# Optimization experiments

Measured on AMD Instinct MI355X. Metric: run time of the kernel, lower is better.

The kernel has to match this reference:

```python
import jax, jax.numpy as jnp
import numpy as np

WIDTH = 64
HEIGHT = 64
FEAT = 128
LAT = 64
NUM_SLOTS = 7


def pixel_coords(img_size):
    g = jnp.linspace(-1.0, 1.0, img_size)
    g1, g2 = jnp.meshgrid(g, g, indexing='ij')  # matches torch.meshgrid default
    return jnp.stack([g1, g2], axis=0)[None]  # (1, 2, S, S)


def clamp_pg(x, lo, hi):
    # clamp that preserves gradients (straight-through)
    return x + jax.lax.stop_gradient(jnp.clip(x, lo, hi) - x)


def setup_inputs() -> dict:
    key = jax.random.key(0)
    k0, k1, k2, k3 = jax.random.split(key, 4)
    bs = 64
    x = jax.random.normal(k0, (bs, FEAT, WIDTH, HEIGHT), jnp.float32)
    rand_pixel = jax.random.uniform(k1, (bs, 1, WIDTH, HEIGHT), jnp.float32)
    conv_w = jax.random.normal(k2, (LAT, FEAT), jnp.float32) / np.sqrt(FEAT)
    conv_b = jax.random.normal(k3, (LAT,), jnp.float32) * 0.01
    gate = jnp.asarray(0.5, jnp.float32)  # ScalarGate parameter (nonzero so c_f is non-degenerate)
    # laplacian kernel: sigma_init = 1 / (sqrt(num_slots) * log 2)
    log_sigma = jnp.asarray(np.log(1.0 / (np.sqrt(NUM_SLOTS) * np.log(2.0))), jnp.float32)
    return {'x': x, 'rand_pixel': rand_pixel, 'conv_w': conv_w, 'conv_b': conv_b,
            'gate': gate, 'log_sigma': log_sigma, 'num_cl_steps': 6}


def _forward(x, rand_pixel, conv_w, conv_b, gate, log_sigma, num_cl_steps):
    bs = x.shape[0]
    # SemiConv: gated 1x1 conv + fixed uv coordinate channels
    out = gate * (jnp.einsum('of,bfhw->bohw', conv_w, x) + conv_b[None, :, None, None])
    uv = jnp.concatenate([jnp.zeros((1, LAT - 2, WIDTH, HEIGHT), out.dtype),
                          pixel_coords(WIDTH).astype(out.dtype)], axis=1)
    c_f = out + uv                      # (bs, LAT, W, H)
    delta = out[:, -2:]                 # (bs, 2, W, H)
    sigma = jnp.exp(log_sigma)
    c_flat = c_f.reshape(bs, LAT, -1)   # (bs, LAT, W*H)
    b_idx = jnp.arange(bs)
    log_s0 = jnp.zeros((bs, 1, WIDTH, HEIGHT), c_f.dtype)

    def step(log_s, _):
        # interpolate-to-same-size is identity -> scope = exp(log_s)
        probs = (rand_pixel * jnp.exp(log_s)).reshape(bs, -1)
        idx = jnp.argmax(probs, axis=1)                 # (bs,)
        seed = c_flat[b_idx, :, idx]                    # (bs, LAT)
        diff = c_f - seed[:, :, None, None]
        dist = jnp.sqrt(clamp_pg((diff ** 2).sum(1), 1e-10, 1e10))  # euclidian (laplacian kernel)
        alpha = jnp.exp(-dist / sigma)[:, None]         # (bs, 1, W, H)
        alpha = clamp_pg(alpha, 0.01, 0.99)
        log_m = log_s + jnp.log(alpha)
        new_log_s = log_s + jnp.log1p(-alpha)
        return new_log_s, (log_m, new_log_s, seed)

    log_s_final, (log_m_steps, log_s_steps, seeds) = jax.lax.scan(
        step, log_s0, None, length=num_cl_steps)
    # log_m_k has num_cl_steps masks plus the final scope appended
    log_m_k = jnp.concatenate([log_m_steps, log_s_final[None]], axis=0)
    log_s_k = jnp.concatenate([log_s0[None], log_s_steps], axis=0)
    return log_m_k, log_s_k, c_f, delta, seeds


def reference(x, rand_pixel, conv_w, conv_b, gate, log_sigma, num_cl_steps):
    return _forward(x, rand_pixel, conv_w, conv_b, gate, log_sigma, num_cl_steps)
```

## Files before the change

### kernel.cpp

```cpp
#include <hip/hip_runtime.h>

#define NPIX 4096
#define FEAT 128
#define LAT 64
#define BS 64
#define NSTEPS 6

#define OFF_LOGM  0u
#define OFF_LOGS  1835008u
#define OFF_CF    3670016u
#define OFF_DELTA 20447232u
#define OFF_SEEDS 20971520u

__device__ __forceinline__ void amax_comb(float& bv, int& bi, float v, int i) {
    if (v > bv || (v == bv && i < bi)) { bv = v; bi = i; }
}

__global__ __launch_bounds__(256, 2) void conv_kernel(
    const float* __restrict__ x, const float* __restrict__ rand_pixel,
    const float* __restrict__ w, const float* __restrict__ bias,
    const float* __restrict__ gate_p, float* __restrict__ out,
    float* __restrict__ pval, int* __restrict__ pidx)
{
    __shared__ float wT[FEAT][68];

    const int tid  = threadIdx.x;
    const int b    = blockIdx.x >> 4;
    const int tile = blockIdx.x & 15;
    const int p0   = tile * 256;
    const int lane = tid & 63;
    const int og   = tid >> 6;

    #pragma unroll
    for (int k = 0; k < 32; ++k) {
        int idx = k * 256 + tid;
        wT[idx & 127][idx >> 7] = w[idx];
    }
    __syncthreads();

    const float gate = gate_p[0];

    float4 acc[16];
    #pragma unroll
    for (int i = 0; i < 16; ++i) acc[i] = make_float4(0.f, 0.f, 0.f, 0.f);

    const float* xb = x + (size_t)b * FEAT * NPIX + p0 + lane * 4;

    #pragma unroll 2
    for (int f = 0; f < FEAT; ++f) {
        float4 xv = *(const float4*)(xb + (size_t)f * NPIX);
        const float* wrow = &wT[f][og * 16];
        #pragma unroll
        for (int oi = 0; oi < 16; oi += 4) {
            float4 wv = *(const float4*)(wrow + oi);
            acc[oi+0].x = fmaf(wv.x, xv.x, acc[oi+0].x);
            acc[oi+0].y = fmaf(wv.x, xv.y, acc[oi+0].y);
            acc[oi+0].z = fmaf(wv.x, xv.z, acc[oi+0].z);
            acc[oi+0].w = fmaf(wv.x, xv.w, acc[oi+0].w);
            acc[oi+1].x = fmaf(wv.y, xv.x, acc[oi+1].x);
            acc[oi+1].y = fmaf(wv.y, xv.y, acc[oi+1].y);
            acc[oi+1].z = fmaf(wv.y, xv.z, acc[oi+1].z);
            acc[oi+1].w = fmaf(wv.y, xv.w, acc[oi+1].w);
            acc[oi+2].x = fmaf(wv.z, xv.x, acc[oi+2].x);
            acc[oi+2].y = fmaf(wv.z, xv.y, acc[oi+2].y);
            acc[oi+2].z = fmaf(wv.z, xv.z, acc[oi+2].z);
            acc[oi+2].w = fmaf(wv.z, xv.w, acc[oi+2].w);
            acc[oi+3].x = fmaf(wv.w, xv.x, acc[oi+3].x);
            acc[oi+3].y = fmaf(wv.w, xv.y, acc[oi+3].y);
            acc[oi+3].z = fmaf(wv.w, xv.z, acc[oi+3].z);
            acc[oi+3].w = fmaf(wv.w, xv.w, acc[oi+3].w);
        }
    }

    const int pbase = p0 + lane * 4;
    float* cf = out + OFF_CF + (size_t)b * LAT * NPIX;

    #pragma unroll
    for (int oi = 0; oi < 16; ++oi) {
        int o = og * 16 + oi;
        float bo = bias[o];
        float4 v;
        v.x = gate * (acc[oi].x + bo);
        v.y = gate * (acc[oi].y + bo);
        v.z = gate * (acc[oi].z + bo);
        v.w = gate * (acc[oi].w + bo);
        if (o >= 62) {
            float* dp = out + OFF_DELTA + ((size_t)b * 2 + (o - 62)) * NPIX + pbase;
            *(float4*)dp = v;
            if (o == 62) {
                float g1 = (float)(-1.0 + 2.0 * (double)(pbase >> 6) / 63.0);
                v.x += g1; v.y += g1; v.z += g1; v.w += g1;
            } else {
                int j = pbase & 63;
                v.x += (float)(-1.0 + 2.0 * (double)(j + 0) / 63.0);
                v.y += (float)(-1.0 + 2.0 * (double)(j + 1) / 63.0);
                v.z += (float)(-1.0 + 2.0 * (double)(j + 2) / 63.0);
                v.w += (float)(-1.0 + 2.0 * (double)(j + 3) / 63.0);
            }
        }
        *(float4*)(cf + (size_t)o * NPIX + pbase) = v;
    }

    if (og == 0) {
        *(float4*)(out + OFF_LOGS + (size_t)b * NPIX + pbase) = make_float4(0.f, 0.f, 0.f, 0.f);

        float4 rv = *(const float4*)(rand_pixel + (size_t)b * NPIX + pbase);
        float bv = rv.x; int bi = pbase;
        if (rv.y > bv) { bv = rv.y; bi = pbase + 1; }
        if (rv.z > bv) { bv = rv.z; bi = pbase + 2; }
        if (rv.w > bv) { bv = rv.w; bi = pbase + 3; }
        #pragma unroll
        for (int off = 32; off > 0; off >>= 1) {
            float ov = __shfl_down(bv, off, 64);
            int   oi2 = __shfl_down(bi, off, 64);
            amax_comb(bv, bi, ov, oi2);
        }
        if (lane == 0) { pval[blockIdx.x] = bv; pidx[blockIdx.x] = bi; }
    }
}

__global__ __launch_bounds__(256, 4) void step_kernel(
    const float* __restrict__ rand_pixel, const float* __restrict__ log_sigma_p,
    float* __restrict__ out, float* __restrict__ pval, int* __restrict__ pidx,
    int step)
{
    __shared__ float s_seed[LAT];
    __shared__ float s_rv[4];
    __shared__ int   s_ri[4];

    const int tid  = threadIdx.x;
    const int b    = blockIdx.x >> 4;
    const int tile = blockIdx.x & 15;
    const int p    = tile * 256 + tid;

    float bv = -1.0f; int bi = 0;
    #pragma unroll
    for (int k = 0; k < 16; ++k) {
        float v = pval[b * 16 + k];
        int  id = pidx[b * 16 + k];
        amax_comb(bv, bi, v, id);
    }

    const float* cf = out + OFF_CF + (size_t)b * LAT * NPIX;
    if (tid < LAT) s_seed[tid] = cf[(size_t)tid * NPIX + bi];
    __syncthreads();

    if (tile == 0 && tid < LAT)
        out[OFF_SEEDS + ((size_t)step * BS + b) * LAT + tid] = s_seed[tid];

    float d2 = 0.f;
    #pragma unroll 16
    for (int c = 0; c < LAT; ++c) {
        float d = cf[(size_t)c * NPIX + p] - s_seed[c];
        d2 = fmaf(d, d, d2);
    }
    float dist  = sqrtf(fminf(fmaxf(d2, 1e-10f), 1e10f));
    float sigma = expf(log_sigma_p[0]);
    float alpha = expf(-dist / sigma);
    alpha = fminf(fmaxf(alpha, 0.01f), 0.99f);

    float ls  = out[OFF_LOGS + ((size_t)step * BS + b) * NPIX + p];
    float lm  = ls + logf(alpha);
    float lsn = ls + log1pf(-alpha);

    out[OFF_LOGM + ((size_t)step * BS + b) * NPIX + p]       = lm;
    out[OFF_LOGS + ((size_t)(step + 1) * BS + b) * NPIX + p] = lsn;
    if (step == NSTEPS - 1)
        out[OFF_LOGM + ((size_t)NSTEPS * BS + b) * NPIX + p] = lsn;

    if (step < NSTEPS - 1) {
        float prob = rand_pixel[(size_t)b * NPIX + p] * expf(lsn);
        int   idx  = p;
        #pragma unroll
        for (int off = 32; off > 0; off >>= 1) {
            float ov = __shfl_down(prob, off, 64);
            int   oi = __shfl_down(idx, off, 64);
            amax_comb(prob, idx, ov, oi);
        }
        int lane = tid & 63, wid = tid >> 6;
        if (lane == 0) { s_rv[wid] = prob; s_ri[wid] = idx; }
        __syncthreads();
        if (tid == 0) {
            float fb = s_rv[0]; int fi = s_ri[0];
            #pragma unroll
            for (int k = 1; k < 4; ++k) amax_comb(fb, fi, s_rv[k], s_ri[k]);
            pval[blockIdx.x] = fb; pidx[blockIdx.x] = fi;
        }
    }
}

extern "C" void kernel_launch(void* const* d_in, const int* in_sizes, int n_in,
                              void* d_out, int out_size, void* d_ws, size_t ws_size,
                              hipStream_t stream) {
    const float* x          = (const float*)d_in[0];
    const float* rand_pixel = (const float*)d_in[1];
    const float* w          = (const float*)d_in[2];
    const float* bias       = (const float*)d_in[3];
    const float* gate       = (const float*)d_in[4];
    const float* log_sigma  = (const float*)d_in[5];

    float* out  = (float*)d_out;
    float* pval = (float*)d_ws;
    int*   pidx = (int*)((char*)d_ws + 1024 * sizeof(float));

    conv_kernel<<<1024, 256, 0, stream>>>(x, rand_pixel, w, bias, gate, out, pval, pidx);
    for (int s = 0; s < NSTEPS; ++s)
        step_kernel<<<1024, 256, 0, stream>>>(rand_pixel, log_sigma, out, pval, pidx, s);
}
```

Baseline: 155.8 us.

## Fuse conv and clustering steps into one cooperative kernel with register-resident features

```diff
diff --git a/kernel.cpp b/kernel.cpp
--- a/kernel.cpp
+++ b/kernel.cpp
@@ -16,175 +16,170 @@
     if (v > bv || (v == bv && i < bi)) { bv = v; bi = i; }
 }
 
-__global__ __launch_bounds__(256, 2) void conv_kernel(
+__global__ void prep(const float* __restrict__ w, const float* __restrict__ bias,
+                     const float* __restrict__ gate_p,
+                     float* __restrict__ gwt, float* __restrict__ gbias,
+                     int* __restrict__ cnt)
+{
+    int i = blockIdx.x * 256 + threadIdx.x;
+    int o = i >> 7, f = i & 127;
+    gwt[f * 64 + o] = gate_p[0] * w[i];
+    if (i < 64)     gbias[i] = gate_p[0] * bias[i];
+    if (i < BS * 8) cnt[i]   = 0;
+}
+
+__global__ __launch_bounds__(512, 4) void fused(
     const float* __restrict__ x, const float* __restrict__ rand_pixel,
-    const float* __restrict__ w, const float* __restrict__ bias,
-    const float* __restrict__ gate_p, float* __restrict__ out,
-    float* __restrict__ pval, int* __restrict__ pidx)
+    const float* __restrict__ log_sigma_p, float* __restrict__ out,
+    const float* __restrict__ gwt, const float* __restrict__ gbias,
+    float* pv, int* pi, int* cnt)
 {
-    __shared__ float wT[FEAT][68];
+    __shared__ float s_mv[8];
+    __shared__ int   s_mi[8];
+    __shared__ __align__(16) float s_seed[LAT];
+    __shared__ float s_rv[8];
+    __shared__ int   s_ri[8];
 
     const int tid  = threadIdx.x;
-    const int b    = blockIdx.x >> 4;
-    const int tile = blockIdx.x & 15;
-    const int p0   = tile * 256;
-    const int lane = tid & 63;
-    const int og   = tid >> 6;
-
+    const int b    = blockIdx.x >> 3;
+    const int tile = blockIdx.x & 7;
+    const int p    = tile * 512 + tid;
+
+    const float* xr = x + (size_t)b * FEAT * NPIX + p;
+
+    float cr[LAT];
     #pragma unroll
-    for (int k = 0; k < 32; ++k) {
-        int idx = k * 256 + tid;
-        wT[idx & 127][idx >> 7] = w[idx];
-    }
-    __syncthreads();
-
-    const float gate = gate_p[0];
-
-    float4 acc[16];
+    for (int c = 0; c < LAT; ++c) cr[c] = gbias[c];
+
+    #pragma unroll 1
+    for (int fc = 0; fc < 8; ++fc) {
+        float xb[16];
+        #pragma unroll
+        for (int i = 0; i < 16; ++i)
+            xb[i] = xr[(size_t)(fc * 16 + i) * NPIX];
+        #pragma unroll
+        for (int f = 0; f < 16; ++f) {
+            const float* wr = gwt + (fc * 16 + f) * 64;
+            const float xv = xb[f];
+            #pragma unroll
+            for (int c = 0; c < LAT; ++c)
+                cr[c] = fmaf(wr[c], xv, cr[c]);
+        }
+    }
+
+    out[OFF_DELTA + ((size_t)b * 2 + 0) * NPIX + p] = cr[62];
+    out[OFF_DELTA + ((size_t)b * 2 + 1) * NPIX + p] = cr[63];
+    cr[62] += (float)(-1.0 + 2.0 * (double)(p >> 6) / 63.0);
+    cr[63] += (float)(-1.0 + 2.0 * (double)(p & 63) / 63.0);
+
+    float* cf = out + OFF_CF + (size_t)b * LAT * NPIX;
     #pragma unroll
-    for (int i = 0; i < 16; ++i) acc[i] = make_float4(0.f, 0.f, 0.f, 0.f);
-
-    const float* xb = x + (size_t)b * FEAT * NPIX + p0 + lane * 4;
-
-    #pragma unroll 2
-    for (int f = 0; f < FEAT; ++f) {
-        float4 xv = *(const float4*)(xb + (size_t)f * NPIX);
-        const float* wrow = &wT[f][og * 16];
-        #pragma unroll
-        for (int oi = 0; oi < 16; oi += 4) {
-            float4 wv = *(const float4*)(wrow + oi);
-            acc[oi+0].x = fmaf(wv.x, xv.x, acc[oi+0].x);
-            acc[oi+0].y = fmaf(wv.x, xv.y, acc[oi+0].y);
-            acc[oi+0].z = fmaf(wv.x, xv.z, acc[oi+0].z);
-            acc[oi+0].w = fmaf(wv.x, xv.w, acc[oi+0].w);
-            acc[oi+1].x = fmaf(wv.y, xv.x, acc[oi+1].x);
-            acc[oi+1].y = fmaf(wv.y, xv.y, acc[oi+1].y);
-            acc[oi+1].z = fmaf(wv.y, xv.z, acc[oi+1].z);
-            acc[oi+1].w = fmaf(wv.y, xv.w, acc[oi+1].w);
-            acc[oi+2].x = fmaf(wv.z, xv.x, acc[oi+2].x);
-            acc[oi+2].y = fmaf(wv.z, xv.y, acc[oi+2].y);
-            acc[oi+2].z = fmaf(wv.z, xv.z, acc[oi+2].z);
-            acc[oi+2].w = fmaf(wv.z, xv.w, acc[oi+2].w);
-            acc[oi+3].x = fmaf(wv.w, xv.x, acc[oi+3].x);
-            acc[oi+3].y = fmaf(wv.w, xv.y, acc[oi+3].y);
-            acc[oi+3].z = fmaf(wv.w, xv.z, acc[oi+3].z);
-            acc[oi+3].w = fmaf(wv.w, xv.w, acc[oi+3].w);
-        }
-    }
-
-    const int pbase = p0 + lane * 4;
-    float* cf = out + OFF_CF + (size_t)b * LAT * NPIX;
-
+    for (int c = 0; c < LAT; ++c) cf[(size_t)c * NPIX + p] = cr[c];
+
+    out[OFF_LOGS + (size_t)b * NPIX + p] = 0.f;
+
+    float cr2 = 0.f;
     #pragma unroll
-    for (int oi = 0; oi < 16; ++oi) {
-        int o = og * 16 + oi;
-        float bo = bias[o];
-        float4 v;
-        v.x = gate * (acc[oi].x + bo);
-        v.y = gate * (acc[oi].y + bo);
-        v.z = gate * (acc[oi].z + bo);
-        v.w = gate * (acc[oi].w + bo);
-        if (o >= 62) {
-            float* dp = out + OFF_DELTA + ((size_t)b * 2 + (o - 62)) * NPIX + pbase;
-            *(float4*)dp = v;
-            if (o == 62) {
-                float g1 = (float)(-1.0 + 2.0 * (double)(pbase >> 6) / 63.0);
-                v.x += g1; v.y += g1; v.z += g1; v.w += g1;
-            } else {
-                int j = pbase & 63;
-                v.x += (float)(-1.0 + 2.0 * (double)(j + 0) / 63.0);
-                v.y += (float)(-1.0 + 2.0 * (double)(j + 1) / 63.0);
-                v.z += (float)(-1.0 + 2.0 * (double)(j + 2) / 63.0);
-                v.w += (float)(-1.0 + 2.0 * (double)(j + 3) / 63.0);
-            }
-        }
-        *(float4*)(cf + (size_t)o * NPIX + pbase) = v;
-    }
-
-    if (og == 0) {
-        *(float4*)(out + OFF_LOGS + (size_t)b * NPIX + pbase) = make_float4(0.f, 0.f, 0.f, 0.f);
-
-        float4 rv = *(const float4*)(rand_pixel + (size_t)b * NPIX + pbase);
-        float bv = rv.x; int bi = pbase;
-        if (rv.y > bv) { bv = rv.y; bi = pbase + 1; }
-        if (rv.z > bv) { bv = rv.z; bi = pbase + 2; }
-        if (rv.w > bv) { bv = rv.w; bi = pbase + 3; }
+    for (int c = 0; c < LAT; ++c) cr2 = fmaf(cr[c], cr[c], cr2);
+
+    const float rp = rand_pixel[(size_t)b * NPIX + p];
+
+    {
+        float bv = rp; int bi = p;
         #pragma unroll
         for (int off = 32; off > 0; off >>= 1) {
             float ov = __shfl_down(bv, off, 64);
-            int   oi2 = __shfl_down(bi, off, 64);
-            amax_comb(bv, bi, ov, oi2);
-        }
-        if (lane == 0) { pval[blockIdx.x] = bv; pidx[blockIdx.x] = bi; }
-    }
-}
-
-__global__ __launch_bounds__(256, 4) void step_kernel(
-    const float* __restrict__ rand_pixel, const float* __restrict__ log_sigma_p,
-    float* __restrict__ out, float* __restrict__ pval, int* __restrict__ pidx,
-    int step)
-{
-    __shared__ float s_seed[LAT];
-    __shared__ float s_rv[4];
-    __shared__ int   s_ri[4];
-
-    const int tid  = threadIdx.x;
-    const int b    = blockIdx.x >> 4;
-    const int tile = blockIdx.x & 15;
-    const int p    = tile * 256 + tid;
-
-    float bv = -1.0f; int bi = 0;
-    #pragma unroll
-    for (int k = 0; k < 16; ++k) {
-        float v = pval[b * 16 + k];
-        int  id = pidx[b * 16 + k];
-        amax_comb(bv, bi, v, id);
-    }
-
-    const float* cf = out + OFF_CF + (size_t)b * LAT * NPIX;
-    if (tid < LAT) s_seed[tid] = cf[(size_t)tid * NPIX + bi];
-    __syncthreads();
-
-    if (tile == 0 && tid < LAT)
-        out[OFF_SEEDS + ((size_t)step * BS + b) * LAT + tid] = s_seed[tid];
-
-    float d2 = 0.f;
-    #pragma unroll 16
-    for (int c = 0; c < LAT; ++c) {
-        float d = cf[(size_t)c * NPIX + p] - s_seed[c];
-        d2 = fmaf(d, d, d2);
-    }
-    float dist  = sqrtf(fminf(fmaxf(d2, 1e-10f), 1e10f));
-    float sigma = expf(log_sigma_p[0]);
-    float alpha = expf(-dist / sigma);
-    alpha = fminf(fmaxf(alpha, 0.01f), 0.99f);
-
-    float ls  = out[OFF_LOGS + ((size_t)step * BS + b) * NPIX + p];
-    float lm  = ls + logf(alpha);
-    float lsn = ls + log1pf(-alpha);
-
-    out[OFF_LOGM + ((size_t)step * BS + b) * NPIX + p]       = lm;
-    out[OFF_LOGS + ((size_t)(step + 1) * BS + b) * NPIX + p] = lsn;
-    if (step == NSTEPS - 1)
-        out[OFF_LOGM + ((size_t)NSTEPS * BS + b) * NPIX + p] = lsn;
-
-    if (step < NSTEPS - 1) {
-        float prob = rand_pixel[(size_t)b * NPIX + p] * expf(lsn);
-        int   idx  = p;
-        #pragma unroll
-        for (int off = 32; off > 0; off >>= 1) {
-            float ov = __shfl_down(prob, off, 64);
-            int   oi = __shfl_down(idx, off, 64);
-            amax_comb(prob, idx, ov, oi);
+            int   oi = __shfl_down(bi, off, 64);
+            amax_comb(bv, bi, ov, oi);
         }
         int lane = tid & 63, wid = tid >> 6;
-        if (lane == 0) { s_rv[wid] = prob; s_ri[wid] = idx; }
+        if (lane == 0) { s_rv[wid] = bv; s_ri[wid] = bi; }
         __syncthreads();
         if (tid == 0) {
             float fb = s_rv[0]; int fi = s_ri[0];
             #pragma unroll
-            for (int k = 1; k < 4; ++k) amax_comb(fb, fi, s_rv[k], s_ri[k]);
-            pval[blockIdx.x] = fb; pidx[blockIdx.x] = fi;
+            for (int k = 1; k < 8; ++k) amax_comb(fb, fi, s_rv[k], s_ri[k]);
+            __hip_atomic_store(&pv[(0 * BS + b) * 8 + tile], fb,
+                               __ATOMIC_RELAXED, __HIP_MEMORY_SCOPE_AGENT);
+            __hip_atomic_store(&pi[(0 * BS + b) * 8 + tile], fi,
+                               __ATOMIC_RELAXED, __HIP_MEMORY_SCOPE_AGENT);
+            __hip_atomic_fetch_add(&cnt[b * 8 + 0], 1,
+                                   __ATOMIC_RELEASE, __HIP_MEMORY_SCOPE_AGENT);
+        }
+    }
+
+    const float sigma = expf(log_sigma_p[0]);
+    float ls = 0.f;
+
+    #pragma unroll 1
+    for (int s = 0; s < NSTEPS; ++s) {
+        if (tid == 0) {
+            while (__hip_atomic_load(&cnt[b * 8 + s], __ATOMIC_ACQUIRE,
+                                     __HIP_MEMORY_SCOPE_AGENT) < 8)
+                __builtin_amdgcn_s_sleep(2);
+        }
+        __syncthreads();
+        if (tid < 8) {
+            s_mv[tid] = __hip_atomic_load(&pv[(s * BS + b) * 8 + tid],
+                                          __ATOMIC_RELAXED, __HIP_MEMORY_SCOPE_AGENT);
+            s_mi[tid] = __hip_atomic_load(&pi[(s * BS + b) * 8 + tid],
+                                          __ATOMIC_RELAXED, __HIP_MEMORY_SCOPE_AGENT);
+        }
+        __syncthreads();
+
+        float bv = -1.0f; int bi = 0;
+        #pragma unroll
+        for (int k = 0; k < 8; ++k) amax_comb(bv, bi, s_mv[k], s_mi[k]);
+
+        if (tid < LAT) s_seed[tid] = cf[(size_t)tid * NPIX + bi];
+        __syncthreads();
+        if (tile == 0 && tid < LAT)
+            out[OFF_SEEDS + ((size_t)s * BS + b) * LAT + tid] = s_seed[tid];
+
+        float dot = 0.f, s2 = 0.f;
+        #pragma unroll
+        for (int c = 0; c < LAT; ++c) {
+            float sv = s_seed[c];
+            dot = fmaf(cr[c], sv, dot);
+            s2  = fmaf(sv, sv, s2);
+        }
+        float d2 = cr2 + s2 - 2.0f * dot;
+
+        float dist  = sqrtf(fminf(fmaxf(d2, 1e-10f), 1e10f));
+        float alpha = expf(-dist / sigma);
+        alpha = fminf(fmaxf(alpha, 0.01f), 0.99f);
+        float lm  = ls + logf(alpha);
+        float lsn = ls + log1pf(-alpha);
+
+        out[OFF_LOGM + ((size_t)s * BS + b) * NPIX + p]       = lm;
+        out[OFF_LOGS + ((size_t)(s + 1) * BS + b) * NPIX + p] = lsn;
+        ls = lsn;
+
+        if (s == NSTEPS - 1) {
+            out[OFF_LOGM + ((size_t)NSTEPS * BS + b) * NPIX + p] = lsn;
+        } else {
+            float prob = rp * expf(lsn);
+            int   idx  = p;
+            #pragma unroll
+            for (int off = 32; off > 0; off >>= 1) {
+                float ov = __shfl_down(prob, off, 64);
+                int   oi = __shfl_down(idx, off, 64);
+                amax_comb(prob, idx, ov, oi);
+            }
+            int lane = tid & 63, wid = tid >> 6;
+            if (lane == 0) { s_rv[wid] = prob; s_ri[wid] = idx; }
+            __syncthreads();
+            if (tid == 0) {
+                float fb = s_rv[0]; int fi = s_ri[0];
+                #pragma unroll
+                for (int k = 1; k < 8; ++k) amax_comb(fb, fi, s_rv[k], s_ri[k]);
+                __hip_atomic_store(&pv[((s + 1) * BS + b) * 8 + tile], fb,
+                                   __ATOMIC_RELAXED, __HIP_MEMORY_SCOPE_AGENT);
+                __hip_atomic_store(&pi[((s + 1) * BS + b) * 8 + tile], fi,
+                                   __ATOMIC_RELAXED, __HIP_MEMORY_SCOPE_AGENT);
+                __hip_atomic_fetch_add(&cnt[b * 8 + s + 1], 1,
+                                       __ATOMIC_RELEASE, __HIP_MEMORY_SCOPE_AGENT);
+            }
         }
     }
 }
@@ -199,11 +194,24 @@
     const float* gate       = (const float*)d_in[4];
     const float* log_sigma  = (const float*)d_in[5];
 
-    float* out  = (float*)d_out;
-    float* pval = (float*)d_ws;
-    int*   pidx = (int*)((char*)d_ws + 1024 * sizeof(float));
-
-    conv_kernel<<<1024, 256, 0, stream>>>(x, rand_pixel, w, bias, gate, out, pval, pidx);
-    for (int s = 0; s < NSTEPS; ++s)
-        step_kernel<<<1024, 256, 0, stream>>>(rand_pixel, log_sigma, out, pval, pidx, s);
-}
+    float* out = (float*)d_out;
+    float* gwt   = (float*)d_ws;
+    float* gbias = (float*)((char*)d_ws + 32768);
+    float* pv    = (float*)((char*)d_ws + 33024);
+    int*   pi    = (int*)((char*)d_ws + 45312);
+    int*   cnt   = (int*)((char*)d_ws + 57600);
+
+    prep<<<32, 256, 0, stream>>>(w, bias, gate, gwt, gbias, cnt);
+
+    const float* a0 = x; const float* a1 = rand_pixel; const float* a2 = log_sigma;
+    float* a3 = out; const float* a4 = gwt; const float* a5 = gbias;
+    float* a6 = pv; int* a7 = pi; int* a8 = cnt;
+    void* kp[9] = {(void*)&a0, (void*)&a1, (void*)&a2, (void*)&a3, (void*)&a4,
+                   (void*)&a5, (void*)&a6, (void*)&a7, (void*)&a8};
+    hipError_t e = hipLaunchCooperativeKernel((const void*)fused,
+                                              dim3(512), dim3(512), kp, 0, stream);
+    if (e != hipSuccess) {
+        fused<<<512, 512, 0, stream>>>(x, rand_pixel, log_sigma, out,
+                                       gwt, gbias, pv, pi, cnt);
+    }
+}
```

New measurement: 218.4 us. 1.4x slower.
